# Kernel optimization log

Hardware: AMD Instinct MI355X
Metric: run time of the kernel (lower is better)

Reference implementation:

```python
import jax, jax.numpy as jnp
import numpy as np

B, NX, NEQ, NINEQ = 1024, 64, 1, 128
NCON = NEQ + NINEQ
MAX_ITERS = 5
INT_REG = 1e-6


def chol_upper(M):
    # upper Cholesky factor U with M = U^T U
    return jnp.swapaxes(jnp.linalg.cholesky(M), -1, -2)


def cho_solve_upper(U, rhs):
    # solve (U^T U) x = rhs, U batched upper triangular
    y = jax.lax.linalg.triangular_solve(U, rhs, left_side=True, lower=False, transpose_a=True)
    return jax.lax.linalg.triangular_solve(U, y, left_side=True, lower=False, transpose_a=False)


def pre_factor_kkt(Q, G, A):
    GT = jnp.swapaxes(G, 1, 2)
    AT = jnp.swapaxes(A, 1, 2)
    U_Q = chol_upper(Q)
    invQ_GT = cho_solve_upper(U_Q, GT)          # [B, nx, nineq]
    R = jnp.matmul(G, invQ_GT)                   # [B, nineq, nineq]
    invQ_AT = cho_solve_upper(U_Q, AT)           # [B, nx, neq]
    A_invQ_AT = jnp.matmul(A, invQ_AT)           # [B, neq, neq]
    U11 = chol_upper(A_invQ_AT)
    G_invQ_AT = jnp.matmul(G, invQ_AT)           # [B, nineq, neq]
    U12 = jax.lax.linalg.triangular_solve(U11, jnp.swapaxes(G_invQ_AT, 1, 2), left_side=True, lower=False)
    U1 = jnp.concatenate((U11, U12), axis=2)     # [B, neq, ncon]
    R = R - jnp.matmul(jnp.swapaxes(U12, 1, 2), U12)
    return U_Q, U1, R


def factor_kkt(U1, R, d):
    # Schur complement factor; d: [B, nineq, 1]
    d_diag = (1.0 / d[..., 0])[:, :, None] * jnp.eye(NINEQ, dtype=d.dtype)[None]
    mat = chol_upper(R + d_diag + INT_REG * jnp.eye(NINEQ, dtype=d.dtype)[None])
    lower = jnp.concatenate((jnp.zeros((B, NINEQ, NEQ), d.dtype), mat), axis=2)
    return jnp.concatenate((U1, lower), axis=1)  # [B, ncon, ncon] upper triangular


def solve_kkt(U_Q, d, G, A, U_S, rx, rs, rz, ry):
    GT = jnp.swapaxes(G, 1, 2)
    AT = jnp.swapaxes(A, 1, 2)
    invQ_rx = cho_solve_upper(U_Q, rx)
    H = jnp.matmul(G, invQ_rx) + rs / d - rz
    H1 = jnp.matmul(A, invQ_rx) - ry
    H = jnp.concatenate((H1, H), axis=1)
    w = -cho_solve_upper(U_S, H)
    w_y = w[:, :NEQ, :]
    w_z = w[:, NEQ:, :]
    g1 = -rx - jnp.matmul(GT, w_z) - jnp.matmul(AT, w_y)
    g2 = -rs - w_z
    dx = cho_solve_upper(U_Q, g1)
    ds = g2 / d
    return dx, ds, w_z, w_y


def get_step(v, dv):
    a = -v / dv
    a = jnp.where(a > 0, a, jnp.inf)
    return jnp.min(a, axis=1)  # [B, 1]


def setup_inputs() -> dict:
    key = jax.random.key(0)
    ks = jax.random.split(key, 6)
    M = jax.random.normal(ks[0], (B, NX, NX), jnp.float32)
    Q = jnp.matmul(M, jnp.swapaxes(M, 1, 2)) / NX + 2.0 * jnp.eye(NX, dtype=jnp.float32)[None]
    p = jax.random.normal(ks[1], (B, NX, 1), jnp.float32)
    A = jax.random.normal(ks[2], (B, NEQ, NX), jnp.float32)
    G = jax.random.normal(ks[3], (B, NINEQ, NX), jnp.float32)
    x0 = jax.random.normal(ks[4], (B, NX, 1), jnp.float32)
    b = jnp.matmul(A, x0)
    h = jnp.matmul(G, x0) + jax.random.uniform(ks[5], (B, NINEQ, 1), jnp.float32) + 0.1
    return {"Q": Q, "p": p, "A": A, "b": b, "G": G, "h": h}


def reference(Q, p, A, b, G, h):
    GT = jnp.swapaxes(G, 1, 2)
    AT = jnp.swapaxes(A, 1, 2)
    U_Q, U1, R = pre_factor_kkt(Q, G, A)

    # primal-dual init
    d0 = jnp.ones((B, NINEQ, 1), Q.dtype)
    U_S0 = factor_kkt(U1, R, d0)
    x, s, z, y = solve_kkt(U_Q, d0, G, A, U_S0, p, jnp.zeros((B, NINEQ, 1), Q.dtype), -h, -b)
    min_s = jnp.min(s, axis=1)  # [B,1]
    min_z = jnp.min(z, axis=1)
    s = s + jnp.where(1.0 - min_s > 1.0, 1.0 - min_s, 0.0)[:, :, None]
    z = z + jnp.where(1.0 - min_z > 1.0, 1.0 - min_z, 0.0)[:, :, None]

    def body(carry, _):
        x, s, z, y = carry
        rx = jnp.matmul(GT, z) + jnp.matmul(Q, x) + p + jnp.matmul(AT, y)
        rs = z
        rz = jnp.matmul(G, x) + s - h
        ry = jnp.matmul(A, x) - b
        mu = jnp.sum(s * z, axis=1) / NINEQ  # [B,1]
        d = z / s
        U_S = factor_kkt(U1, R, d)
        dxa, dsa, dza, dya = solve_kkt(U_Q, d, G, A, U_S, rx, rs, rz, ry)
        alpha = 0.999 * jnp.minimum(jnp.minimum(get_step(z, dza), get_step(s, dsa)), 1.0)[:, :, None]
        s_p = s + alpha * dsa
        z_p = z + alpha * dza
        sig = (jnp.sum(s_p * z_p, axis=1) / jnp.sum(s * z, axis=1)) ** 3
        mu_sig = (-mu * sig)[:, :, None]
        non_zero = (mu_sig + dsa * dza) / s
        dxc, dsc, dzc, dyc = solve_kkt(U_Q, d, G, A, U_S, rx * 0, non_zero, rz * 0, ry * 0)
        dx, ds, dz, dy = dxa + dxc, dsa + dsc, dza + dzc, dya + dyc
        alpha = 0.999 * jnp.minimum(jnp.minimum(get_step(z, dz), get_step(s, ds)), 1.0)[:, :, None]
        return (x + alpha * dx, s + alpha * ds, z + alpha * dz, y + alpha * dy), None

    (x, s, z, y), _ = jax.lax.scan(body, (x, s, z, y), None, length=MAX_ITERS)
    return x
```

## Files before the change

kernel.cpp:

```cpp
#include <hip/hip_runtime.h>
#include <math.h>


#define NT  512
#define T1_O  4352
#define T1_ST 130
#define GP_O  2048
#define QP_O  4352

struct __align__(16) Smem {
  float pool[12672];
  float x[64], rxv[64], t[64], dxa[64];
  float s[128], z[128], rz[128], dsa[128], dza[128], u12[128], dd[128], H[128], Y[128];
  float scalbuf[64];
  float scal[16];
};
static_assert(sizeof(Smem) <= 65536, "LDS must be under 64 KiB for 2 blocks/CU");

enum { SC_H1 = 2, SC_U11I = 4, SC_RY = 5, SC_MU = 6,
       SC_MUSIG = 8, SC_Y = 9, SC_DYA = 10, SC_WY = 11 };

__device__ __forceinline__ float wred_sum(float v) {
#pragma unroll
  for (int off = 32; off > 0; off >>= 1) v += __shfl_down(v, off);
  return v;
}
__device__ __forceinline__ float wred_min(float v) {
#pragma unroll
  for (int off = 32; off > 0; off >>= 1) v = fminf(v, __shfl_down(v, off));
  return v;
}
__device__ __forceinline__ float step_val(float v, float dv) {
  float a = -v / dv;
  return (a > 0.0f) ? a : __builtin_inff();
}
__device__ __forceinline__ constexpr int pk16(int i) {
  return i * 16 - ((i * (i - 1)) >> 1);
}


template<int RW>
__device__ __forceinline__ void elim_publish(Smem& sm, float* pan, float (&Wt)[4][8],
                                             int q, int tc) {
  const int tcd = q >> 1;
  const int co = (q & 1) << 2;
  float L10 = 0, L20 = 0, L30 = 0, L21 = 0, L31 = 0, L32 = 0;
  float id0 = 0, id1 = 0, id2 = 0, id3 = 0;
  if (tc == tcd) {
    float D[4][4];
#pragma unroll
    for (int m = 0; m < 4; ++m)
#pragma unroll
      for (int c = 0; c < 4; ++c) D[m][c] = Wt[m][co + c];
    id0 = 1.0f / D[0][0];
    L10 = D[0][1] * id0; L20 = D[0][2] * id0; L30 = D[0][3] * id0;
#pragma unroll
    for (int c = 0; c < 4; ++c) {
      D[1][c] -= L10 * D[0][c]; D[2][c] -= L20 * D[0][c]; D[3][c] -= L30 * D[0][c];
    }
    id1 = 1.0f / D[1][1];
    L21 = D[1][2] * id1; L31 = D[1][3] * id1;
#pragma unroll
    for (int c = 0; c < 4; ++c) { D[2][c] -= L21 * D[1][c]; D[3][c] -= L31 * D[1][c]; }
    id2 = 1.0f / D[2][2];
    L32 = D[2][3] * id2;
#pragma unroll
    for (int c = 0; c < 4; ++c) D[3][c] -= L32 * D[2][c];
    id3 = 1.0f / D[3][3];
  }
  const int src = ((q & 3) << 4) + tcd;
  L10 = __shfl(L10, src); L20 = __shfl(L20, src); L30 = __shfl(L30, src);
  L21 = __shfl(L21, src); L31 = __shfl(L31, src); L32 = __shfl(L32, src);
#pragma unroll
  for (int c = 0; c < 8; ++c) {
    Wt[1][c] = fmaf(-L10, Wt[0][c], Wt[1][c]);
    Wt[2][c] = fmaf(-L20, Wt[0][c], Wt[2][c]);
    Wt[2][c] = fmaf(-L21, Wt[1][c], Wt[2][c]);
    Wt[3][c] = fmaf(-L30, Wt[0][c], Wt[3][c]);
    Wt[3][c] = fmaf(-L31, Wt[1][c], Wt[3][c]);
    Wt[3][c] = fmaf(-L32, Wt[2][c], Wt[3][c]);
  }
  const int pb = (q >> 1) & 1;
  float* pp = pan + pb * (8 * RW) + (q & 1) * (4 * RW);
  const int j0 = tc << 3;
#pragma unroll
  for (int m = 0; m < 4; ++m) {
    *(float4*)&pp[m * RW + j0]     = make_float4(Wt[m][0], Wt[m][1], Wt[m][2], Wt[m][3]);
    *(float4*)&pp[m * RW + j0 + 4] = make_float4(Wt[m][4], Wt[m][5], Wt[m][6], Wt[m][7]);
  }
  if (tc == tcd) {
    float* sb = sm.scalbuf + pb * 8 + ((q & 1) << 2);
    sb[0] = id0; sb[1] = id1; sb[2] = id2; sb[3] = id3;
    sm.Y[(q << 2) + 0] = id0; sm.Y[(q << 2) + 1] = id1;
    sm.Y[(q << 2) + 2] = id2; sm.Y[(q << 2) + 3] = id3;
  }
}

template<int RW>
__device__ __forceinline__ void apply_panel4(Smem& sm, float* pan, float (&Wt)[4][8],
                                             int pb, int half, int i0, int j0) {
  const float* pp = pan + pb * (8 * RW) + half * (4 * RW);
  const float* sb = sm.scalbuf + pb * 8 + (half << 2);
#pragma unroll 1
  for (int mm = 0; mm < 4; ++mm) {
    const float idm = sb[mm];
    const float4 pv  = *(const float4*)&pp[mm * RW + i0];
    const float4 pj0 = *(const float4*)&pp[mm * RW + j0];
    const float4 pj1 = *(const float4*)&pp[mm * RW + j0 + 4];
    const float um0 = pv.x * idm, um1 = pv.y * idm;
    const float um2 = pv.z * idm, um3 = pv.w * idm;
    const float pjv[8] = {pj0.x, pj0.y, pj0.z, pj0.w, pj1.x, pj1.y, pj1.z, pj1.w};
#pragma unroll
    for (int c = 0; c < 8; ++c) {
      Wt[0][c] = fmaf(-um0, pjv[c], Wt[0][c]);
      Wt[1][c] = fmaf(-um1, pjv[c], Wt[1][c]);
      Wt[2][c] = fmaf(-um2, pjv[c], Wt[2][c]);
      Wt[3][c] = fmaf(-um3, pjv[c], Wt[3][c]);
    }
  }
}

template<int N, int RW, int ST>
__device__ void chol_rank8(Smem& sm, float* pan, float (&Wt)[4][8], int act, int tid) {
  const int tr = tid >> 4, tc = tid & 15;
  const int i0 = tr << 2, j0 = tc << 3;
  constexpr int NP = N / 8;
#pragma unroll 1
  for (int P = 0; P < NP; ++P) {
    const int pb = P & 1;
    if (P > 0 && act && tr >= 2 * P) {
      apply_panel4<RW>(sm, pan, Wt, pb ^ 1, 0, i0, j0);
      apply_panel4<RW>(sm, pan, Wt, pb ^ 1, 1, i0, j0);
    }
    if ((tid >> 6) == (P >> 1)) {
      if (act && tr == 2 * P) elim_publish<RW>(sm, pan, Wt, 2 * P, tc);
      __threadfence_block();
      if (act && tr == 2 * P + 1) {
        apply_panel4<RW>(sm, pan, Wt, pb, 0, i0, j0);
        elim_publish<RW>(sm, pan, Wt, 2 * P + 1, tc);
      }
    }
    __syncthreads();
  }
}

template<int ST>
__device__ __forceinline__ void write_U(Smem& sm, float (&Wt)[4][8], int act,
                                        int i0, int j0) {
  if (act && j0 + 7 >= i0) {
    float sqv[4];
#pragma unroll
    for (int m = 0; m < 4; ++m) sqv[m] = sqrtf(sm.Y[i0 + m]);
    if (j0 >= i0 + 3) {
#pragma unroll
      for (int m = 0; m < 4; ++m)
#pragma unroll
        for (int qq = 0; qq < 4; ++qq)
          *(float2*)&sm.pool[(i0 + m) * ST + j0 + 2 * qq] =
              make_float2(Wt[m][2 * qq] * sqv[m], Wt[m][2 * qq + 1] * sqv[m]);
    } else {
#pragma unroll
      for (int m = 0; m < 4; ++m) {
        const int i = i0 + m;
#pragma unroll
        for (int c = 0; c < 8; ++c) {
          const int j = j0 + c;
          if (j >= i) sm.pool[i * ST + j] = Wt[m][c] * sqv[m];
        }
      }
    }
  }
}

template<int N, int ST>
__device__ void trtri_fast(Smem& sm, float* vd, int tid) {
  constexpr int NB = N >> 4;
  if (tid < NB * 16) {
    const int blk = tid >> 4, c = tid & 15;
    const float* D = sm.pool + (blk << 4) * ST + (blk << 4);
    float vv[16];
#pragma unroll
    for (int i = 15; i >= 0; --i) {
      float acc = 0.0f;
      for (int k = i + 1; k < 16; ++k) acc += D[i * ST + k] * vv[k];
      const float di = D[i * ST + i];
      const float val = (i == c) ? (1.0f / di) : (-acc / di);
      vv[i] = (i <= c) ? val : 0.0f;
    }
#pragma unroll
    for (int i = 0; i < 16; ++i)
      if (i <= c) vd[blk * 136 + pk16(i) + (c - i)] = vv[i];
  }
  __syncthreads();
  constexpr int NROWS = 16 * (NB * (NB - 1) / 2);
  if (tid < NROWS) {
    int J = 1, base = 0;
    while (base + 16 * J <= tid) { base += 16 * J; ++J; }
    const int k = tid - base, Jb = J << 4;
    float u[16], o[16];
    float2* wr = (float2*)&sm.pool[k * ST + Jb];
#pragma unroll
    for (int q = 0; q < 8; ++q) { const float2 v = wr[q]; u[2*q] = v.x; u[2*q+1] = v.y; }
    const float* vdj = vd + J * 136;
#pragma unroll
    for (int c = 0; c < 16; ++c) {
      float acc = 0.0f;
#pragma unroll
      for (int jj = 0; jj <= c; ++jj) acc += u[jj] * vdj[pk16(jj) + (c - jj)];
      o[c] = acc;
    }
#pragma unroll
    for (int q = 0; q < 8; ++q) wr[q] = make_float2(o[2*q], o[2*q+1]);
  } else {
    for (int idx = tid - NROWS; idx < 256; idx += NT - NROWS) {
      const int r = idx >> 4, c2 = idx & 15;
      if (c2 >= r) sm.pool[r * ST + c2] = vd[pk16(r) + (c2 - r)];
    }
  }
  for (int J = 1; J < NB; ++J) {
    __syncthreads();
    const int Jb = J << 4;
    const int nStrip = Jb << 2;
    float acc[4] = {0.0f, 0.0f, 0.0f, 0.0f};
    int wi = 0, wc = 0;
    if (tid < nStrip) {
      wi = tid >> 2; wc = (tid & 3) << 2;
      for (int k = wi; k < Jb; ++k) {
        const float v = sm.pool[wi * ST + k];
        const float2 u0 = *(const float2*)&sm.pool[k * ST + Jb + wc];
        const float2 u1 = *(const float2*)&sm.pool[k * ST + Jb + wc + 2];
        acc[0] = fmaf(v, u0.x, acc[0]); acc[1] = fmaf(v, u0.y, acc[1]);
        acc[2] = fmaf(v, u1.x, acc[2]); acc[3] = fmaf(v, u1.y, acc[3]);
      }
      acc[0] = -acc[0]; acc[1] = -acc[1]; acc[2] = -acc[2]; acc[3] = -acc[3];
    } else if (tid < nStrip + 64) {
      const int l = tid - nStrip;
      const int r = l >> 2; wi = Jb + r; wc = (l & 3) << 2;
      const float* vp = vd + J * 136 + pk16(r) - r;
#pragma unroll
      for (int q = 0; q < 4; ++q) {
        const int c = wc + q;
        acc[q] = (c >= r) ? vp[c] : 0.0f;
      }
    }
    __syncthreads();
    if (tid < nStrip) {
      *(float2*)&sm.pool[wi * ST + Jb + wc]     = make_float2(acc[0], acc[1]);
      *(float2*)&sm.pool[wi * ST + Jb + wc + 2] = make_float2(acc[2], acc[3]);
    } else if (tid < nStrip + 64) {
      const int r = wi - Jb;
#pragma unroll
      for (int q = 0; q < 4; ++q)
        if (wc + q >= r) sm.pool[wi * ST + Jb + wc + q] = acc[q];
    }
  }
  __syncthreads();
}


__device__ __forceinline__ void elim_sweep(Smem& sm, float (&Wt)[4][8],
                                           int q, int tc) {
  const int tcd = q >> 1;
  const int co = (q & 1) << 2;
  float L10 = 0, L20 = 0, L30 = 0, L21 = 0, L31 = 0, L32 = 0;
  float id0 = 0, id1 = 0, id2 = 0, id3 = 0;
  if (tc == tcd) {
    float D[4][4];
#pragma unroll
    for (int m = 0; m < 4; ++m)
#pragma unroll
      for (int c = 0; c < 4; ++c) D[m][c] = Wt[m][co + c];
    id0 = 1.0f / D[0][0];
    L10 = D[0][1] * id0; L20 = D[0][2] * id0; L30 = D[0][3] * id0;
#pragma unroll
    for (int c = 0; c < 4; ++c) {
      D[1][c] -= L10 * D[0][c]; D[2][c] -= L20 * D[0][c]; D[3][c] -= L30 * D[0][c];
    }
    id1 = 1.0f / D[1][1];
    L21 = D[1][2] * id1; L31 = D[1][3] * id1;
#pragma unroll
    for (int c = 0; c < 4; ++c) { D[2][c] -= L21 * D[1][c]; D[3][c] -= L31 * D[1][c]; }
    id2 = 1.0f / D[2][2];
    L32 = D[2][3] * id2;
#pragma unroll
    for (int c = 0; c < 4; ++c) D[3][c] -= L32 * D[2][c];
    id3 = 1.0f / D[3][3];
  }
  const int src = ((q & 3) << 4) + tcd;
  L10 = __shfl(L10, src); L20 = __shfl(L20, src); L30 = __shfl(L30, src);
  L21 = __shfl(L21, src); L31 = __shfl(L31, src); L32 = __shfl(L32, src);
  id0 = __shfl(id0, src); id1 = __shfl(id1, src);
  id2 = __shfl(id2, src); id3 = __shfl(id3, src);
#pragma unroll
  for (int c = 0; c < 8; ++c) {
    Wt[1][c] = fmaf(-L10, Wt[0][c], Wt[1][c]);
    Wt[2][c] = fmaf(-L20, Wt[0][c], Wt[2][c]);
    Wt[2][c] = fmaf(-L21, Wt[1][c], Wt[2][c]);
    Wt[3][c] = fmaf(-L30, Wt[0][c], Wt[3][c]);
    Wt[3][c] = fmaf(-L31, Wt[1][c], Wt[3][c]);
    Wt[3][c] = fmaf(-L32, Wt[2][c], Wt[3][c]);
  }
  const int pb = (q >> 1) & 1;
  float* pp = sm.pool + pb * 1024 + (q & 1) * 512;
  const int j0 = tc << 3;
#pragma unroll
  for (int m = 0; m < 4; ++m) {
    *(float4*)&pp[m * 128 + j0]     = make_float4(Wt[m][0], Wt[m][1], Wt[m][2], Wt[m][3]);
    *(float4*)&pp[m * 128 + j0 + 4] = make_float4(Wt[m][4], Wt[m][5], Wt[m][6], Wt[m][7]);
  }
  if (tc == tcd) {
    float* sb = sm.scalbuf + 16 + pb * 24 + (q & 1) * 12;
    sb[0] = id0; sb[1] = id1; sb[2] = id2; sb[3] = id3;
    sb[4] = L10; sb[5] = L20; sb[6] = L30; sb[7] = L21; sb[8] = L31; sb[9] = L32;
  }
#pragma unroll
  for (int c = 0; c < 8; ++c) {
    const float t3 = id3 * Wt[3][c];
    const float t2 = id2 * Wt[2][c] - L32 * t3;
    const float t1v = id1 * Wt[1][c] - L21 * t2 - L31 * t3;
    const float t0 = id0 * Wt[0][c] - L10 * t1v - L20 * t2 - L30 * t3;
    Wt[0][c] = t0; Wt[1][c] = t1v; Wt[2][c] = t2; Wt[3][c] = t3;
  }
  if (tc == tcd) {
    const float m10 = -L10, m21 = -L21, m32 = -L32;
    const float m20 = -L20 + L21 * L10;
    const float m31 = -L31 + L32 * L21;
    const float m30 = -L30 + L31 * L10 + L32 * L20 - L32 * L21 * L10;
    const float P00 = id0 + id1*m10*m10 + id2*m20*m20 + id3*m30*m30;
    const float P01 = id1*m10 + id2*m20*m21 + id3*m30*m31;
    const float P02 = id2*m20 + id3*m30*m32;
    const float P03 = id3*m30;
    const float P11 = id1 + id2*m21*m21 + id3*m31*m31;
    const float P12 = id2*m21 + id3*m31*m32;
    const float P13 = id3*m31;
    const float P22 = id2 + id3*m32*m32;
    const float P23 = id3*m32;
    const float P33 = id3;
    Wt[0][co+0] = -P00; Wt[0][co+1] = -P01; Wt[0][co+2] = -P02; Wt[0][co+3] = -P03;
    Wt[1][co+0] = -P01; Wt[1][co+1] = -P11; Wt[1][co+2] = -P12; Wt[1][co+3] = -P13;
    Wt[2][co+0] = -P02; Wt[2][co+1] = -P12; Wt[2][co+2] = -P22; Wt[2][co+3] = -P23;
    Wt[3][co+0] = -P03; Wt[3][co+1] = -P13; Wt[3][co+2] = -P23; Wt[3][co+3] = -P33;
  }
}

__device__ __forceinline__ void apply_sweep(Smem& sm, float (&Wt)[4][8],
                                            int q, int i0, int j0, int tr, int tc,
                                            int skip_partner) {
  if (tr == q) return;
  if (skip_partner && !(q & 1) && tr == q + 1) return;
  const int pb = (q >> 1) & 1;
  const float* pp = sm.pool + pb * 1024 + (q & 1) * 512;
  const float* sb = sm.scalbuf + 16 + pb * 24 + (q & 1) * 12;
#pragma unroll 1
  for (int mm = 0; mm < 4; ++mm) {
    const float idm = sb[mm];
    const float4 pv  = *(const float4*)&pp[mm * 128 + i0];
    const float4 pj0 = *(const float4*)&pp[mm * 128 + j0];
    const float4 pj1 = *(const float4*)&pp[mm * 128 + j0 + 4];
    const float um0 = pv.x * idm, um1 = pv.y * idm;
    const float um2 = pv.z * idm, um3 = pv.w * idm;
    const float pjv[8] = {pj0.x, pj0.y, pj0.z, pj0.w, pj1.x, pj1.y, pj1.z, pj1.w};
#pragma unroll
    for (int c = 0; c < 8; ++c) {
      Wt[0][c] = fmaf(-um0, pjv[c], Wt[0][c]);
      Wt[1][c] = fmaf(-um1, pjv[c], Wt[1][c]);
      Wt[2][c] = fmaf(-um2, pjv[c], Wt[2][c]);
      Wt[3][c] = fmaf(-um3, pjv[c], Wt[3][c]);
    }
  }
  if (tc == (q >> 1)) {
    const int co = (q & 1) << 2;
    const float id0 = sb[0], id1 = sb[1], id2 = sb[2], id3 = sb[3];
    const float L10 = sb[4], L20 = sb[5], L30 = sb[6];
    const float L21 = sb[7], L31 = sb[8], L32 = sb[9];
#pragma unroll
    for (int r = 0; r < 4; ++r) {
      const float f0 = pp[0 * 128 + i0 + r];
      const float f1 = pp[1 * 128 + i0 + r];
      const float f2 = pp[2 * 128 + i0 + r];
      const float f3 = pp[3 * 128 + i0 + r];
      const float t3 = id3 * f3;
      const float t2 = id2 * f2 - L32 * t3;
      const float t1v = id1 * f1 - L21 * t2 - L31 * t3;
      const float t0 = id0 * f0 - L10 * t1v - L20 * t2 - L30 * t3;
      Wt[r][co+0] = t0; Wt[r][co+1] = t1v; Wt[r][co+2] = t2; Wt[r][co+3] = t3;
    }
  }
}

__device__ void sweep128(Smem& sm, float (&Wt)[4][8], int tid) {
  const int tr = tid >> 4, tc = tid & 15;
  const int i0 = tr << 2, j0 = tc << 3;
#pragma unroll 1
  for (int P = 0; P < 16; ++P) {
    if (P > 0) {
      apply_sweep(sm, Wt, 2 * P - 2, i0, j0, tr, tc, 1);
      apply_sweep(sm, Wt, 2 * P - 1, i0, j0, tr, tc, 1);
    }
    if ((tid >> 6) == (P >> 1)) {
      if (tr == 2 * P) elim_sweep(sm, Wt, 2 * P, tc);
      __threadfence_block();
      if (tr == 2 * P + 1) {
        apply_sweep(sm, Wt, 2 * P, i0, j0, tr, tc, 0);
        elim_sweep(sm, Wt, 2 * P + 1, tc);
      }
    }
    __syncthreads();
  }
  apply_sweep(sm, Wt, 30, i0, j0, tr, tc, 1);
  apply_sweep(sm, Wt, 31, i0, j0, tr, tc, 1);
}

__device__ void rebuild_S(Smem& sm, float (&Wt)[4][8], int init, int tid) {
  const int tr = tid >> 4, tc = tid & 15;
  const int i0 = tr << 2, j0 = tc << 3;
#pragma unroll
  for (int m = 0; m < 4; ++m)
#pragma unroll
    for (int c = 0; c < 8; ++c) Wt[m][c] = 0.0f;
#pragma unroll 2
  for (int k = 0; k < 64; ++k) {
    const float4 a  = *(const float4*)&sm.pool[T1_O + k * T1_ST + i0];
    const float4 b0 = *(const float4*)&sm.pool[T1_O + k * T1_ST + j0];
    const float4 b1 = *(const float4*)&sm.pool[T1_O + k * T1_ST + j0 + 4];
    const float av[4] = {a.x, a.y, a.z, a.w};
    const float bv[8] = {b0.x, b0.y, b0.z, b0.w, b1.x, b1.y, b1.z, b1.w};
#pragma unroll
    for (int m = 0; m < 4; ++m)
#pragma unroll
      for (int c = 0; c < 8; ++c) Wt[m][c] = fmaf(av[m], bv[c], Wt[m][c]);
  }
#pragma unroll
  for (int m = 0; m < 4; ++m) {
    const float ui = sm.u12[i0 + m];
#pragma unroll
    for (int c = 0; c < 8; ++c) Wt[m][c] -= ui * sm.u12[j0 + c];
  }
#pragma unroll
  for (int m = 0; m < 4; ++m) {
    const int i = i0 + m;
    if (i >= j0 && i < j0 + 8) {
      const int c = i - j0;
      const float dval = init ? 1.0f : sm.s[i] / sm.z[i];
      Wt[m][c] = Wt[m][c] + dval + 1e-6f;
    }
  }
}

__device__ void solve_kkt(Smem& sm, const float (&Wt)[4][8], const float* qreg,
                          const float* Gb, const float* Ab,
                          int has_rx, const float* rx, const float* rs,
                          int has_rz, const float* rz, float ry,
                          float* dx_t, float* ds_t, float* dz_t, int dy_slot,
                          int accum, int tid) {
  const float u11i = sm.scal[SC_U11I];
  const int o8 = tid >> 3, seg = tid & 7;
  const int tr = tid >> 4, tc = tid & 15;
  const int i0 = tr << 2, j0 = tc << 3;
  if (has_rx) {
    {
      float acc = 0.0f;
#pragma unroll
      for (int c = 0; c < 8; ++c) acc += qreg[c] * rx[seg * 8 + c];
      acc += __shfl_down(acc, 4); acc += __shfl_down(acc, 2); acc += __shfl_down(acc, 1);
      if (seg == 0) sm.t[o8] = acc;
    }
    __syncthreads();
    {
      const int i = tid >> 2, q = tid & 3;
      float acc = 0.0f;
      const float* gr = Gb + (i << 6) + (q << 4);
#pragma unroll
      for (int kk = 0; kk < 16; kk += 4) {
        const float4 g4 = *(const float4*)(gr + kk);
        const float4 t4 = *(const float4*)&sm.t[(q << 4) + kk];
        acc += g4.x * t4.x + g4.y * t4.y + g4.z * t4.z + g4.w * t4.w;
      }
      float h1v = (tid < 64) ? Ab[tid] * sm.t[tid] : 0.0f;
      h1v = wred_sum(h1v);
      acc += __shfl_down(acc, 2); acc += __shfl_down(acc, 1);
      if (q == 0) {
        if (rs) acc += rs[i] / sm.dd[i];
        if (has_rz) acc -= rz[i];
        sm.H[i] = acc;
      }
      if (tid == 0) sm.scal[SC_H1] = h1v - ry;
    }
    __syncthreads();
  }
  const float y1 = sm.scal[SC_H1] * u11i;
  {
    float v[8];
#pragma unroll
    for (int c = 0; c < 8; ++c) v[c] = sm.H[j0 + c] - sm.u12[j0 + c] * y1;
#pragma unroll
    for (int m = 0; m < 4; ++m) {
      float p = 0.0f;
#pragma unroll
      for (int c = 0; c < 8; ++c) p = fmaf(Wt[m][c], v[c], p);
      p += __shfl_down(p, 8); p += __shfl_down(p, 4);
      p += __shfl_down(p, 2); p += __shfl_down(p, 1);
      if (tc == 0) sm.Y[i0 + m] = p;
    }
  }
  __syncthreads();
  if (tid < 256) {
    const int o = tid & 63, p = tid >> 6;
    float acc = 0.0f;
    for (int i = (p << 5); i < (p << 5) + 32; ++i)
      acc -= Gb[(i << 6) + o] * sm.Y[i];
    sm.pool[GP_O + (p << 6) + o] = acc;
  } else if (tid < 384) {
    const int i = tid - 256;
    const float wzv = sm.Y[i];
    const float r = rs ? rs[i] : 0.0f;
    const float dsv = (-r - wzv) / sm.dd[i];
    if (accum) { ds_t[i] += dsv; dz_t[i] += wzv; }
    else       { ds_t[i] = dsv;  dz_t[i] = wzv; }
  } else if (tid < 448) {
    const int l = tid - 384;
    float vv = sm.u12[l] * sm.Y[l] + sm.u12[l + 64] * sm.Y[l + 64];
    vv = wred_sum(vv);
    if (l == 0) {
      const float wyv = -(y1 + vv) * u11i;
      if (accum) sm.scal[dy_slot] += wyv; else sm.scal[dy_slot] = wyv;
      sm.scal[SC_WY] = wyv;
    }
  }
  __syncthreads();
  const float wy = sm.scal[SC_WY];
  {
    float acc = 0.0f;
#pragma unroll
    for (int c = 0; c < 8; ++c) {
      const int j = seg * 8 + c;
      float g1v = sm.pool[GP_O + j] + sm.pool[GP_O + 64 + j] + sm.pool[GP_O + 128 + j]
                + sm.pool[GP_O + 192 + j] - Ab[j] * wy;
      if (has_rx) g1v -= rx[j];
      acc += qreg[c] * g1v;
    }
    acc += __shfl_down(acc, 4); acc += __shfl_down(acc, 2); acc += __shfl_down(acc, 1);
    if (seg == 0) { if (accum) dx_t[o8] += acc; else dx_t[o8] = acc; }
  }
  __syncthreads();
}

__global__ __launch_bounds__(NT, 4)
void optnet_kernel(const float* __restrict__ Qg, const float* __restrict__ pg,
                   const float* __restrict__ Ag, const float* __restrict__ bg,
                   const float* __restrict__ Gg, const float* __restrict__ hg,
                   float* __restrict__ outg) {
  __shared__ Smem sm;
  const int bId = blockIdx.x;
  const int tid = threadIdx.x;
  const float* Qb = Qg + (size_t)bId * 4096;
  const float* pb = pg + (size_t)bId * 64;
  const float* Ab = Ag + (size_t)bId * 64;
  const float  bb = bg[bId];
  const float* Gb = Gg + (size_t)bId * 8192;
  const float* hb = hg + (size_t)bId * 128;

  for (int idx = tid; idx < 4096; idx += NT)
    sm.pool[(idx >> 6) * 68 + (idx & 63)] = Qb[idx];
  if (tid < 128) sm.dd[tid] = 1.0f;
  __syncthreads();
  {
    const int tr = tid >> 4, tc = tid & 15;
    const int i0 = tr << 2, j0 = tc << 3;
    const int act = (tr < 16) && (tc < 8);
    float Wq[4][8];
    if (act) {
#pragma unroll
      for (int m = 0; m < 4; ++m)
#pragma unroll
        for (int c = 0; c < 8; ++c)
          Wq[m][c] = sm.pool[(i0 + m) * 68 + j0 + c];
    }
    chol_rank8<64, 64, 68>(sm, sm.pool + QP_O, Wq, act, tid);
    write_U<68>(sm, Wq, act, i0, j0);
  }
  __syncthreads();
  trtri_fast<64, 68>(sm, sm.pool + QP_O, tid);
  for (int idx = tid; idx < 4096; idx += NT) {
    const int i = idx >> 6, j = idx & 63;
    if (i > j) sm.pool[i * 68 + j] = 0.0f;
  }
  __syncthreads();
  float qreg[8];
  {
    const int o = tid >> 3, sgq = tid & 7;
#pragma unroll 1
    for (int c = 0; c < 8; ++c) {
      const int j = sgq * 8 + c;
      float acc = 0.0f;
      for (int k = 0; k < 64; ++k) acc += sm.pool[o * 68 + k] * sm.pool[j * 68 + k];
      qreg[c] = acc;
    }
  }
  if (tid < 64) {
    float acc = 0.0f;
    for (int m = 0; m < 64; ++m) acc += sm.pool[m * 68 + tid] * Ab[m];
    sm.t[tid] = acc;
  }
  __syncthreads();
  if (tid < 64) {
    float v = sm.t[tid] * sm.t[tid];
    v = wred_sum(v);
    if (tid == 0) sm.scal[SC_U11I] = 1.0f / sqrtf(v);
  }
  __syncthreads();
  {
    const int kt = tid & 15, jt = tid >> 4;
    const int k0 = kt << 2, j0 = jt << 2;
    float t1a[4][4] = {};
#pragma unroll 1
    for (int m = 0; m < 64; m += 4) {
      const float4 g0 = *(const float4*)&Gb[(j0 + 0) * 64 + m];
      const float4 g1 = *(const float4*)&Gb[(j0 + 1) * 64 + m];
      const float4 g2 = *(const float4*)&Gb[(j0 + 2) * 64 + m];
      const float4 g3 = *(const float4*)&Gb[(j0 + 3) * 64 + m];
      const float gr[4][4] = {{g0.x, g0.y, g0.z, g0.w}, {g1.x, g1.y, g1.z, g1.w},
                              {g2.x, g2.y, g2.z, g2.w}, {g3.x, g3.y, g3.z, g3.w}};
#pragma unroll
      for (int i = 0; i < 4; ++i) {
        const float4 v = *(const float4*)&sm.pool[(m + i) * 68 + k0];
        const float vv[4] = {v.x, v.y, v.z, v.w};
#pragma unroll
        for (int a = 0; a < 4; ++a)
#pragma unroll
          for (int b2 = 0; b2 < 4; ++b2)
            t1a[a][b2] = fmaf(vv[a], gr[b2][i], t1a[a][b2]);
      }
    }
#pragma unroll
    for (int a = 0; a < 4; ++a)
      *(float4*)&sm.pool[T1_O + (k0 + a) * T1_ST + j0] =
          make_float4(t1a[a][0], t1a[a][1], t1a[a][2], t1a[a][3]);
  }
  __syncthreads();
  {
    const int o = tid & 127, p = tid >> 7;
    float acc = 0.0f;
    for (int k = (p << 4); k < (p << 4) + 16; ++k)
      acc += sm.pool[T1_O + k * T1_ST + o] * sm.t[k];
    sm.pool[(p << 7) + o] = acc;
  }
  __syncthreads();
  if (tid < 128) {
    sm.u12[tid] = (sm.pool[tid] + sm.pool[128 + tid] + sm.pool[256 + tid] + sm.pool[384 + tid])
                  * sm.scal[SC_U11I];
  } else if (tid < 256) {
    sm.rz[tid - 128] = -hb[tid - 128];
  }
  __syncthreads();

  float Wt[4][8];

  rebuild_S(sm, Wt, 1, tid);
  sweep128(sm, Wt, tid);
  solve_kkt(sm, Wt, qreg, Gb, Ab, 1, pb, nullptr, 1, sm.rz, -bb,
            sm.x, sm.s, sm.z, SC_Y, 0, tid);
  if (tid < 64) {
    float v = fminf(sm.s[tid], sm.s[tid + 64]);
    v = wred_min(v);
    v = __shfl(v, 0);
    const float cs = 1.0f - v;
    if (cs > 1.0f) { sm.s[tid] += cs; sm.s[tid + 64] += cs; }
  } else if (tid < 128) {
    const int l = tid - 64;
    float v = fminf(sm.z[l], sm.z[l + 64]);
    v = wred_min(v);
    v = __shfl(v, 0);
    const float cz = 1.0f - v;
    if (cz > 1.0f) { sm.z[l] += cz; sm.z[l + 64] += cz; }
  }
  __syncthreads();

  for (int it = 0; it < 5; ++it) {
    if (tid < 256) {
      const int o = tid & 63, pq = tid >> 6;
      float acc = 0.0f;
      for (int i = (pq << 5); i < (pq << 5) + 32; ++i) acc += Gb[(i << 6) + o] * sm.z[i];
      for (int k = (pq << 4); k < (pq << 4) + 16; ++k) acc += Qb[(k << 6) + o] * sm.x[k];
      sm.pool[GP_O + (pq << 6) + o] = acc;
    } else {
      const int l = tid - 256, i = l >> 1, q = l & 1;
      const float* gr = Gb + (i << 6) + (q << 5);
      float acc = 0.0f;
#pragma unroll
      for (int kk = 0; kk < 32; kk += 4) {
        const float4 g4 = *(const float4*)(gr + kk);
        const float4 x4 = *(const float4*)&sm.x[(q << 5) + kk];
        acc += g4.x * x4.x + g4.y * x4.y + g4.z * x4.z + g4.w * x4.w;
      }
      acc += __shfl_down(acc, 1);
      if (q == 0) sm.rz[i] = acc + sm.s[i] - hb[i];
    }
    __syncthreads();
    if (tid < 64) {
      sm.rxv[tid] = pb[tid] + Ab[tid] * sm.scal[SC_Y]
                  + sm.pool[GP_O + tid] + sm.pool[GP_O + 64 + tid]
                  + sm.pool[GP_O + 128 + tid] + sm.pool[GP_O + 192 + tid];
    } else if (tid < 128) {
      const int l = tid - 64;
      float v = Ab[l] * sm.x[l];
      v = wred_sum(v);
      if (l == 0) sm.scal[SC_RY] = v - bb;
    } else if (tid < 192) {
      const int l = tid - 128;
      float v = sm.s[l] * sm.z[l] + sm.s[l + 64] * sm.z[l + 64];
      v = wred_sum(v);
      if (l == 0) sm.scal[SC_MU] = v * (1.0f / 128.0f);
    } else if (tid < 320) {
      const int i = tid - 192;
      sm.dd[i] = sm.z[i] / sm.s[i];
    }
    __syncthreads();
    rebuild_S(sm, Wt, 0, tid);
    sweep128(sm, Wt, tid);
    solve_kkt(sm, Wt, qreg, Gb, Ab, 1, sm.rxv, sm.z, 1, sm.rz, sm.scal[SC_RY],
              sm.dxa, sm.dsa, sm.dza, SC_DYA, 0, tid);
    if (tid < 64) {
      float m = __builtin_inff();
#pragma unroll
      for (int rep = 0; rep < 2; ++rep) {
        const int i = tid + 64 * rep;
        m = fminf(m, step_val(sm.z[i], sm.dza[i]));
        m = fminf(m, step_val(sm.s[i], sm.dsa[i]));
      }
      m = wred_min(m);
      float alpha = 0.999f * fminf(m, 1.0f);
      alpha = __shfl(alpha, 0);
      float v = 0.0f;
#pragma unroll
      for (int rep = 0; rep < 2; ++rep) {
        const int i = tid + 64 * rep;
        v += (sm.s[i] + alpha * sm.dsa[i]) * (sm.z[i] + alpha * sm.dza[i]);
      }
      v = wred_sum(v);
      if (tid == 0) {
        const float mu = sm.scal[SC_MU];
        const float r = v / (mu * 128.0f);
        sm.scal[SC_MUSIG] = -mu * r * r * r;
      }
    }
    __syncthreads();
    if (tid < 128) {
      const float v = (sm.scal[SC_MUSIG] + sm.dsa[tid] * sm.dza[tid]) / sm.s[tid];
      sm.rz[tid] = v;
      sm.H[tid] = v / sm.dd[tid];
    } else if (tid == 128) {
      sm.scal[SC_H1] = 0.0f;
    }
    __syncthreads();
    solve_kkt(sm, Wt, qreg, Gb, Ab, 0, nullptr, sm.rz, 0, nullptr, 0.0f,
              sm.dxa, sm.dsa, sm.dza, SC_DYA, 1, tid);
    if (tid < 64) {
      float m = __builtin_inff();
#pragma unroll
      for (int rep = 0; rep < 2; ++rep) {
        const int i = tid + 64 * rep;
        m = fminf(m, step_val(sm.z[i], sm.dza[i]));
        m = fminf(m, step_val(sm.s[i], sm.dsa[i]));
      }
      m = wred_min(m);
      float a2 = 0.999f * fminf(m, 1.0f);
      a2 = __shfl(a2, 0);
      sm.s[tid]      += a2 * sm.dsa[tid];
      sm.s[tid + 64] += a2 * sm.dsa[tid + 64];
      sm.z[tid]      += a2 * sm.dza[tid];
      sm.z[tid + 64] += a2 * sm.dza[tid + 64];
      sm.x[tid]      += a2 * sm.dxa[tid];
      if (tid == 0) sm.scal[SC_Y] += a2 * sm.scal[SC_DYA];
    }
    __syncthreads();
  }
  if (tid < 64) outg[((size_t)bId << 6) + tid] = sm.x[tid];
}

extern "C" void kernel_launch(void* const* d_in, const int* in_sizes, int n_in,
                              void* d_out, int out_size, void* d_ws, size_t ws_size,
                              hipStream_t stream) {
  (void)n_in; (void)d_ws; (void)ws_size; (void)out_size;
  const float* Q = (const float*)d_in[0];
  const float* p = (const float*)d_in[1];
  const float* A = (const float*)d_in[2];
  const float* b = (const float*)d_in[3];
  const float* G = (const float*)d_in[4];
  const float* h = (const float*)d_in[5];
  const int B = in_sizes[3];
  optnet_kernel<<<B, NT, 0, stream>>>(Q, p, A, b, G, h, (float*)d_out);
}
```

Baseline: 1.991 ms.

## Shrink LDS footprint by aliasing vectors into pool and permuting panel layout

Moves the per-problem vectors (s, z, rz, dsa, dza, u12, dd, H, Y, x, rxv, dxa) into unused regions of the shared pool and drops the padded T1 row stride, cutting LDS to about 50 KB so three blocks can fit per CU; launch bounds are raised accordingly. The panel and T1 storage use a permuted column-chunk layout (pch) with a 128 stride, so float4 reads stay bank-conflict-light without padding. The goal is more resident blocks to hide latency. Risks are register pressure under the tighter launch bound and aliasing bugs if the pool regions overlap live data.

```diff
diff --git a/kernel.cpp b/kernel.cpp
--- a/kernel.cpp
+++ b/kernel.cpp
@@ -2,20 +2,31 @@
 #include <math.h>
 
 
-#define NT  512
-#define T1_O  4352
-#define T1_ST 130
-#define GP_O  2048
-#define QP_O  4352
+#define NT 512
+#define T1_O 4352
+#define GP_O 2048
+#define QP_O 4352
+
+#define SM_S   (sm.pool + 2304)
+#define SM_Z   (sm.pool + 2432)
+#define SM_RZ  (sm.pool + 2560)
+#define SM_DSA (sm.pool + 2688)
+#define SM_DZA (sm.pool + 2816)
+#define SM_U12 (sm.pool + 2944)
+#define SM_DD  (sm.pool + 3072)
+#define SM_H   (sm.pool + 3200)
+#define SM_Y   (sm.pool + 3328)
+#define SM_X   (sm.pool + 3456)
+#define SM_RXV (sm.pool + 3520)
+#define SM_DXA (sm.pool + 3584)
 
 struct __align__(16) Smem {
-  float pool[12672];
-  float x[64], rxv[64], t[64], dxa[64];
-  float s[128], z[128], rz[128], dsa[128], dza[128], u12[128], dd[128], H[128], Y[128];
+  float pool[12544];
+  float t[64];
   float scalbuf[64];
   float scal[16];
 };
-static_assert(sizeof(Smem) <= 65536, "LDS must be under 64 KiB for 2 blocks/CU");
+static_assert(sizeof(Smem) <= 52000, "LDS must allow 3 blocks/CU");
 
 enum { SC_H1 = 2, SC_U11I = 4, SC_RY = 5, SC_MU = 6,
        SC_MUSIG = 8, SC_Y = 9, SC_DYA = 10, SC_WY = 11 };
@@ -36,6 +47,9 @@
 }
 __device__ __forceinline__ constexpr int pk16(int i) {
   return i * 16 - ((i * (i - 1)) >> 1);
+}
+__device__ __forceinline__ constexpr int pch(int c) {
+  return ((c & 1) << 4) | (c >> 1);
 }
 
 
@@ -91,8 +105,8 @@
   if (tc == tcd) {
     float* sb = sm.scalbuf + pb * 8 + ((q & 1) << 2);
     sb[0] = id0; sb[1] = id1; sb[2] = id2; sb[3] = id3;
-    sm.Y[(q << 2) + 0] = id0; sm.Y[(q << 2) + 1] = id1;
-    sm.Y[(q << 2) + 2] = id2; sm.Y[(q << 2) + 3] = id3;
+    sm.t[(q << 2) + 0] = id0; sm.t[(q << 2) + 1] = id1;
+    sm.t[(q << 2) + 2] = id2; sm.t[(q << 2) + 3] = id3;
   }
 }
 
@@ -150,7 +164,7 @@
   if (act && j0 + 7 >= i0) {
     float sqv[4];
 #pragma unroll
-    for (int m = 0; m < 4; ++m) sqv[m] = sqrtf(sm.Y[i0 + m]);
+    for (int m = 0; m < 4; ++m) sqv[m] = sqrtf(sm.t[i0 + m]);
     if (j0 >= i0 + 3) {
 #pragma unroll
       for (int m = 0; m < 4; ++m)
@@ -302,11 +316,11 @@
   }
   const int pb = (q >> 1) & 1;
   float* pp = sm.pool + pb * 1024 + (q & 1) * 512;
-  const int j0 = tc << 3;
+  const int c0 = tc << 2;
 #pragma unroll
   for (int m = 0; m < 4; ++m) {
-    *(float4*)&pp[m * 128 + j0]     = make_float4(Wt[m][0], Wt[m][1], Wt[m][2], Wt[m][3]);
-    *(float4*)&pp[m * 128 + j0 + 4] = make_float4(Wt[m][4], Wt[m][5], Wt[m][6], Wt[m][7]);
+    *(float4*)&pp[m * 128 + c0]      = make_float4(Wt[m][0], Wt[m][1], Wt[m][2], Wt[m][3]);
+    *(float4*)&pp[m * 128 + 64 + c0] = make_float4(Wt[m][4], Wt[m][5], Wt[m][6], Wt[m][7]);
   }
   if (tc == tcd) {
     float* sb = sm.scalbuf + 16 + pb * 24 + (q & 1) * 12;
@@ -351,12 +365,14 @@
   const int pb = (q >> 1) & 1;
   const float* pp = sm.pool + pb * 1024 + (q & 1) * 512;
   const float* sb = sm.scalbuf + 16 + pb * 24 + (q & 1) * 12;
+  const int c0 = tc << 2;
+  const int pvo = pch(tr) << 2;
 #pragma unroll 1
   for (int mm = 0; mm < 4; ++mm) {
     const float idm = sb[mm];
-    const float4 pv  = *(const float4*)&pp[mm * 128 + i0];
-    const float4 pj0 = *(const float4*)&pp[mm * 128 + j0];
-    const float4 pj1 = *(const float4*)&pp[mm * 128 + j0 + 4];
+    const float4 pv  = *(const float4*)&pp[mm * 128 + pvo];
+    const float4 pj0 = *(const float4*)&pp[mm * 128 + c0];
+    const float4 pj1 = *(const float4*)&pp[mm * 128 + 64 + c0];
     const float um0 = pv.x * idm, um1 = pv.y * idm;
     const float um2 = pv.z * idm, um3 = pv.w * idm;
     const float pjv[8] = {pj0.x, pj0.y, pj0.z, pj0.w, pj1.x, pj1.y, pj1.z, pj1.w};
@@ -375,10 +391,10 @@
     const float L21 = sb[7], L31 = sb[8], L32 = sb[9];
 #pragma unroll
     for (int r = 0; r < 4; ++r) {
-      const float f0 = pp[0 * 128 + i0 + r];
-      const float f1 = pp[1 * 128 + i0 + r];
-      const float f2 = pp[2 * 128 + i0 + r];
-      const float f3 = pp[3 * 128 + i0 + r];
+      const float f0 = pp[0 * 128 + pvo + r];
+      const float f1 = pp[1 * 128 + pvo + r];
+      const float f2 = pp[2 * 128 + pvo + r];
+      const float f3 = pp[3 * 128 + pvo + r];
       const float t3 = id3 * f3;
       const float t2 = id2 * f2 - L32 * t3;
       const float t1v = id1 * f1 - L21 * t2 - L31 * t3;
@@ -414,15 +430,18 @@
 __device__ void rebuild_S(Smem& sm, float (&Wt)[4][8], int init, int tid) {
   const int tr = tid >> 4, tc = tid & 15;
   const int i0 = tr << 2, j0 = tc << 3;
+  const int c0 = tc << 2;
+  const int pvo = pch(tr) << 2;
 #pragma unroll
   for (int m = 0; m < 4; ++m)
 #pragma unroll
     for (int c = 0; c < 8; ++c) Wt[m][c] = 0.0f;
 #pragma unroll 2
   for (int k = 0; k < 64; ++k) {
-    const float4 a  = *(const float4*)&sm.pool[T1_O + k * T1_ST + i0];
-    const float4 b0 = *(const float4*)&sm.pool[T1_O + k * T1_ST + j0];
-    const float4 b1 = *(const float4*)&sm.pool[T1_O + k * T1_ST + j0 + 4];
+    const float* row = sm.pool + T1_O + k * 128;
+    const float4 a  = *(const float4*)&row[pvo];
+    const float4 b0 = *(const float4*)&row[c0];
+    const float4 b1 = *(const float4*)&row[64 + c0];
     const float av[4] = {a.x, a.y, a.z, a.w};
     const float bv[8] = {b0.x, b0.y, b0.z, b0.w, b1.x, b1.y, b1.z, b1.w};
 #pragma unroll
@@ -432,16 +451,16 @@
   }
 #pragma unroll
   for (int m = 0; m < 4; ++m) {
-    const float ui = sm.u12[i0 + m];
-#pragma unroll
-    for (int c = 0; c < 8; ++c) Wt[m][c] -= ui * sm.u12[j0 + c];
+    const float ui = SM_U12[i0 + m];
+#pragma unroll
+    for (int c = 0; c < 8; ++c) Wt[m][c] -= ui * SM_U12[j0 + c];
   }
 #pragma unroll
   for (int m = 0; m < 4; ++m) {
     const int i = i0 + m;
     if (i >= j0 && i < j0 + 8) {
       const int c = i - j0;
-      const float dval = init ? 1.0f : sm.s[i] / sm.z[i];
+      const float dval = init ? 1.0f : SM_S[i] / SM_Z[i];
       Wt[m][c] = Wt[m][c] + dval + 1e-6f;
     }
   }
@@ -480,9 +499,9 @@
       h1v = wred_sum(h1v);
       acc += __shfl_down(acc, 2); acc += __shfl_down(acc, 1);
       if (q == 0) {
-        if (rs) acc += rs[i] / sm.dd[i];
+        if (rs) acc += rs[i] / SM_DD[i];
         if (has_rz) acc -= rz[i];
-        sm.H[i] = acc;
+        SM_H[i] = acc;
       }
       if (tid == 0) sm.scal[SC_H1] = h1v - ry;
     }
@@ -492,7 +511,7 @@
   {
     float v[8];
 #pragma unroll
-    for (int c = 0; c < 8; ++c) v[c] = sm.H[j0 + c] - sm.u12[j0 + c] * y1;
+    for (int c = 0; c < 8; ++c) v[c] = SM_H[j0 + c] - SM_U12[j0 + c] * y1;
 #pragma unroll
     for (int m = 0; m < 4; ++m) {
       float p = 0.0f;
@@ -500,7 +519,7 @@
       for (int c = 0; c < 8; ++c) p = fmaf(Wt[m][c], v[c], p);
       p += __shfl_down(p, 8); p += __shfl_down(p, 4);
       p += __shfl_down(p, 2); p += __shfl_down(p, 1);
-      if (tc == 0) sm.Y[i0 + m] = p;
+      if (tc == 0) SM_Y[i0 + m] = p;
     }
   }
   __syncthreads();
@@ -508,18 +527,18 @@
     const int o = tid & 63, p = tid >> 6;
     float acc = 0.0f;
     for (int i = (p << 5); i < (p << 5) + 32; ++i)
-      acc -= Gb[(i << 6) + o] * sm.Y[i];
+      acc -= Gb[(i << 6) + o] * SM_Y[i];
     sm.pool[GP_O + (p << 6) + o] = acc;
   } else if (tid < 384) {
     const int i = tid - 256;
-    const float wzv = sm.Y[i];
+    const float wzv = SM_Y[i];
     const float r = rs ? rs[i] : 0.0f;
-    const float dsv = (-r - wzv) / sm.dd[i];
+    const float dsv = (-r - wzv) / SM_DD[i];
     if (accum) { ds_t[i] += dsv; dz_t[i] += wzv; }
     else       { ds_t[i] = dsv;  dz_t[i] = wzv; }
   } else if (tid < 448) {
     const int l = tid - 384;
-    float vv = sm.u12[l] * sm.Y[l] + sm.u12[l + 64] * sm.Y[l + 64];
+    float vv = SM_U12[l] * SM_Y[l] + SM_U12[l + 64] * SM_Y[l + 64];
     vv = wred_sum(vv);
     if (l == 0) {
       const float wyv = -(y1 + vv) * u11i;
@@ -545,7 +564,7 @@
   __syncthreads();
 }
 
-__global__ __launch_bounds__(NT, 4)
+__global__ __launch_bounds__(NT, 6)
 void optnet_kernel(const float* __restrict__ Qg, const float* __restrict__ pg,
                    const float* __restrict__ Ag, const float* __restrict__ bg,
                    const float* __restrict__ Gg, const float* __restrict__ hg,
@@ -562,7 +581,6 @@
 
   for (int idx = tid; idx < 4096; idx += NT)
     sm.pool[(idx >> 6) * 68 + (idx & 63)] = Qb[idx];
-  if (tid < 128) sm.dd[tid] = 1.0f;
   __syncthreads();
   {
     const int tr = tid >> 4, tc = tid & 15;
@@ -612,6 +630,7 @@
   {
     const int kt = tid & 15, jt = tid >> 4;
     const int k0 = kt << 2, j0 = jt << 2;
+    const int woff = pch(jt) << 2;
     float t1a[4][4] = {};
 #pragma unroll 1
     for (int m = 0; m < 64; m += 4) {
@@ -634,23 +653,27 @@
     }
 #pragma unroll
     for (int a = 0; a < 4; ++a)
-      *(float4*)&sm.pool[T1_O + (k0 + a) * T1_ST + j0] =
+      *(float4*)&sm.pool[T1_O + (k0 + a) * 128 + woff] =
           make_float4(t1a[a][0], t1a[a][1], t1a[a][2], t1a[a][3]);
   }
   __syncthreads();
   {
     const int o = tid & 127, p = tid >> 7;
+    const int oc = o >> 2;
+    const int ooff = (pch(oc) << 2) | (o & 3);
     float acc = 0.0f;
     for (int k = (p << 4); k < (p << 4) + 16; ++k)
-      acc += sm.pool[T1_O + k * T1_ST + o] * sm.t[k];
+      acc += sm.pool[T1_O + k * 128 + ooff] * sm.t[k];
     sm.pool[(p << 7) + o] = acc;
   }
   __syncthreads();
   if (tid < 128) {
-    sm.u12[tid] = (sm.pool[tid] + sm.pool[128 + tid] + sm.pool[256 + tid] + sm.pool[384 + tid])
+    SM_U12[tid] = (sm.pool[tid] + sm.pool[128 + tid] + sm.pool[256 + tid] + sm.pool[384 + tid])
                   * sm.scal[SC_U11I];
   } else if (tid < 256) {
-    sm.rz[tid - 128] = -hb[tid - 128];
+    SM_RZ[tid - 128] = -hb[tid - 128];
+  } else if (tid < 384) {
+    SM_DD[tid - 256] = 1.0f;
   }
   __syncthreads();
 
@@ -658,21 +681,21 @@
 
   rebuild_S(sm, Wt, 1, tid);
   sweep128(sm, Wt, tid);
-  solve_kkt(sm, Wt, qreg, Gb, Ab, 1, pb, nullptr, 1, sm.rz, -bb,
-            sm.x, sm.s, sm.z, SC_Y, 0, tid);
+  solve_kkt(sm, Wt, qreg, Gb, Ab, 1, pb, nullptr, 1, SM_RZ, -bb,
+            SM_X, SM_S, SM_Z, SC_Y, 0, tid);
   if (tid < 64) {
-    float v = fminf(sm.s[tid], sm.s[tid + 64]);
+    float v = fminf(SM_S[tid], SM_S[tid + 64]);
     v = wred_min(v);
     v = __shfl(v, 0);
     const float cs = 1.0f - v;
-    if (cs > 1.0f) { sm.s[tid] += cs; sm.s[tid + 64] += cs; }
+    if (cs > 1.0f) { SM_S[tid] += cs; SM_S[tid + 64] += cs; }
   } else if (tid < 128) {
     const int l = tid - 64;
-    float v = fminf(sm.z[l], sm.z[l + 64]);
+    float v = fminf(SM_Z[l], SM_Z[l + 64]);
     v = wred_min(v);
     v = __shfl(v, 0);
     const float cz = 1.0f - v;
-    if (cz > 1.0f) { sm.z[l] += cz; sm.z[l + 64] += cz; }
+    if (cz > 1.0f) { SM_Z[l] += cz; SM_Z[l + 64] += cz; }
   }
   __syncthreads();
 
@@ -680,8 +703,8 @@
     if (tid < 256) {
       const int o = tid & 63, pq = tid >> 6;
       float acc = 0.0f;
-      for (int i = (pq << 5); i < (pq << 5) + 32; ++i) acc += Gb[(i << 6) + o] * sm.z[i];
-      for (int k = (pq << 4); k < (pq << 4) + 16; ++k) acc += Qb[(k << 6) + o] * sm.x[k];
+      for (int i = (pq << 5); i < (pq << 5) + 32; ++i) acc += Gb[(i << 6) + o] * SM_Z[i];
+      for (int k = (pq << 4); k < (pq << 4) + 16; ++k) acc += Qb[(k << 6) + o] * SM_X[k];
       sm.pool[GP_O + (pq << 6) + o] = acc;
     } else {
       const int l = tid - 256, i = l >> 1, q = l & 1;
@@ -690,43 +713,43 @@
 #pragma unroll
       for (int kk = 0; kk < 32; kk += 4) {
         const float4 g4 = *(const float4*)(gr + kk);
-        const float4 x4 = *(const float4*)&sm.x[(q << 5) + kk];
+        const float4 x4 = *(const float4*)&SM_X[(q << 5) + kk];
         acc += g4.x * x4.x + g4.y * x4.y + g4.z * x4.z + g4.w * x4.w;
       }
       acc += __shfl_down(acc, 1);
-      if (q == 0) sm.rz[i] = acc + sm.s[i] - hb[i];
+      if (q == 0) SM_RZ[i] = acc + SM_S[i] - hb[i];
     }
     __syncthreads();
     if (tid < 64) {
-      sm.rxv[tid] = pb[tid] + Ab[tid] * sm.scal[SC_Y]
+      SM_RXV[tid] = pb[tid] + Ab[tid] * sm.scal[SC_Y]
                   + sm.pool[GP_O + tid] + sm.pool[GP_O + 64 + tid]
                   + sm.pool[GP_O + 128 + tid] + sm.pool[GP_O + 192 + tid];
     } else if (tid < 128) {
       const int l = tid - 64;
-      float v = Ab[l] * sm.x[l];
+      float v = Ab[l] * SM_X[l];
       v = wred_sum(v);
       if (l == 0) sm.scal[SC_RY] = v - bb;
     } else if (tid < 192) {
       const int l = tid - 128;
-      float v = sm.s[l] * sm.z[l] + sm.s[l + 64] * sm.z[l + 64];
+      float v = SM_S[l] * SM_Z[l] + SM_S[l + 64] * SM_Z[l + 64];
       v = wred_sum(v);
       if (l == 0) sm.scal[SC_MU] = v * (1.0f / 128.0f);
     } else if (tid < 320) {
       const int i = tid - 192;
-      sm.dd[i] = sm.z[i] / sm.s[i];
+      SM_DD[i] = SM_Z[i] / SM_S[i];
     }
     __syncthreads();
     rebuild_S(sm, Wt, 0, tid);
     sweep128(sm, Wt, tid);
-    solve_kkt(sm, Wt, qreg, Gb, Ab, 1, sm.rxv, sm.z, 1, sm.rz, sm.scal[SC_RY],
-              sm.dxa, sm.dsa, sm.dza, SC_DYA, 0, tid);
+    solve_kkt(sm, Wt, qreg, Gb, Ab, 1, SM_RXV, SM_Z, 1, SM_RZ, sm.scal[SC_RY],
+              SM_DXA, SM_DSA, SM_DZA, SC_DYA, 0, tid);
     if (tid < 64) {
       float m = __builtin_inff();
 #pragma unroll
       for (int rep = 0; rep < 2; ++rep) {
         const int i = tid + 64 * rep;
-        m = fminf(m, step_val(sm.z[i], sm.dza[i]));
-        m = fminf(m, step_val(sm.s[i], sm.dsa[i]));
+        m = fminf(m, step_val(SM_Z[i], SM_DZA[i]));
+        m = fminf(m, step_val(SM_S[i], SM_DSA[i]));
       }
       m = wred_min(m);
       float alpha = 0.999f * fminf(m, 1.0f);
@@ -735,7 +758,7 @@
 #pragma unroll
       for (int rep = 0; rep < 2; ++rep) {
         const int i = tid + 64 * rep;
-        v += (sm.s[i] + alpha * sm.dsa[i]) * (sm.z[i] + alpha * sm.dza[i]);
+        v += (SM_S[i] + alpha * SM_DSA[i]) * (SM_Z[i] + alpha * SM_DZA[i]);
       }
       v = wred_sum(v);
       if (tid == 0) {
@@ -746,36 +769,36 @@
     }
     __syncthreads();
     if (tid < 128) {
-      const float v = (sm.scal[SC_MUSIG] + sm.dsa[tid] * sm.dza[tid]) / sm.s[tid];
-      sm.rz[tid] = v;
-      sm.H[tid] = v / sm.dd[tid];
+      const float v = (sm.scal[SC_MUSIG] + SM_DSA[tid] * SM_DZA[tid]) / SM_S[tid];
+      SM_RZ[tid] = v;
+      SM_H[tid] = v / SM_DD[tid];
     } else if (tid == 128) {
       sm.scal[SC_H1] = 0.0f;
     }
     __syncthreads();
-    solve_kkt(sm, Wt, qreg, Gb, Ab, 0, nullptr, sm.rz, 0, nullptr, 0.0f,
-              sm.dxa, sm.dsa, sm.dza, SC_DYA, 1, tid);
+    solve_kkt(sm, Wt, qreg, Gb, Ab, 0, nullptr, SM_RZ, 0, nullptr, 0.0f,
+              SM_DXA, SM_DSA, SM_DZA, SC_DYA, 1, tid);
     if (tid < 64) {
       float m = __builtin_inff();
 #pragma unroll
       for (int rep = 0; rep < 2; ++rep) {
         const int i = tid + 64 * rep;
-        m = fminf(m, step_val(sm.z[i], sm.dza[i]));
-        m = fminf(m, step_val(sm.s[i], sm.dsa[i]));
+        m = fminf(m, step_val(SM_Z[i], SM_DZA[i]));
+        m = fminf(m, step_val(SM_S[i], SM_DSA[i]));
       }
       m = wred_min(m);
       float a2 = 0.999f * fminf(m, 1.0f);
       a2 = __shfl(a2, 0);
-      sm.s[tid]      += a2 * sm.dsa[tid];
-      sm.s[tid + 64] += a2 * sm.dsa[tid + 64];
-      sm.z[tid]      += a2 * sm.dza[tid];
-      sm.z[tid + 64] += a2 * sm.dza[tid + 64];
-      sm.x[tid]      += a2 * sm.dxa[tid];
+      SM_S[tid]      += a2 * SM_DSA[tid];
+      SM_S[tid + 64] += a2 * SM_DSA[tid + 64];
+      SM_Z[tid]      += a2 * SM_DZA[tid];
+      SM_Z[tid + 64] += a2 * SM_DZA[tid + 64];
+      SM_X[tid]      += a2 * SM_DXA[tid];
       if (tid == 0) sm.scal[SC_Y] += a2 * sm.scal[SC_DYA];
     }
     __syncthreads();
   }
-  if (tid < 64) outg[((size_t)bId << 6) + tid] = sm.x[tid];
+  if (tid < 64) outg[((size_t)bId << 6) + tid] = SM_X[tid];
 }
 
 extern "C" void kernel_launch(void* const* d_in, const int* in_sizes, int n_in,
```

Result: slower. 5.549 ms (+178.7%).
